# Kernel tuning notes

Hardware: AMD Instinct MI355X
Metric: run time of the kernel (lower is better)

## Reference

```python
import jax, jax.numpy as jnp
import numpy as np

N_NODES = 100000


def setup_inputs() -> dict:
    key = jax.random.key(0)
    k1, k2, k3, k4 = jax.random.split(key, 4)
    E = 1600000
    in_dim, out_dim = 256, 64
    h = jax.random.normal(k1, (N_NODES, in_dim), dtype=jnp.float32)
    src = jax.random.randint(k2, (E,), 0, N_NODES, dtype=jnp.int64)
    dst = jax.random.randint(k3, (E,), 0, N_NODES, dtype=jnp.int64)
    W = jax.random.normal(k4, (in_dim, out_dim), dtype=jnp.float32) * (1.0 / np.sqrt(in_dim))
    b = jnp.zeros((out_dim,), dtype=jnp.float32)
    return {"h": h, "src": src, "dst": dst, "W": W, "b": b}


def reference(h, src, dst, W, b):
    # dgl GraphConv, norm='both': out = D_in^{-1/2} A D_out^{-1/2} h W + b
    E = src.shape[0]
    ones = jnp.ones((E,), dtype=h.dtype)
    deg_out = jax.ops.segment_sum(ones, src, num_segments=N_NODES)  # out-degree of src nodes
    deg_in = jax.ops.segment_sum(ones, dst, num_segments=N_NODES)   # in-degree of dst nodes
    norm_src = jnp.clip(deg_out, 1.0, None) ** -0.5                  # [N]
    norm_dst = jnp.clip(deg_in, 1.0, None) ** -0.5                   # [N]
    # in_dim > out_dim: project first (as dgl does), then aggregate small features
    x = (h * norm_src[:, None]) @ W                                  # [N, out_dim]
    msgs = x[src]                                                    # [E, out_dim] gather
    agg = jax.ops.segment_sum(msgs, dst, num_segments=N_NODES)      # [N, out_dim] scatter-add
    out = agg * norm_dst[:, None] + b
    # ReLU; dropout is identity in eval mode
    return jax.nn.relu(out)
```

## Files before the change

kernel.cpp:

```cpp
#include <hip/hip_runtime.h>
#include <hip/hip_fp16.h>

#define N_NODES 100000
#define IN_DIM 256
#define OUT_DIM 64
#define NT 782
#define NB 256
#define SCHUNK 4096
#define SB ((NT * NB + SCHUNK - 1) / SCHUNK)
#define SCAN_M (NT * NB)

typedef _Float16 half8 __attribute__((ext_vector_type(8)));
typedef float f32x4 __attribute__((ext_vector_type(4)));

__global__ __launch_bounds__(256) void count_kernel(const int* __restrict__ src,
                                                    const int* __restrict__ dst,
                                                    int* __restrict__ CD, int* __restrict__ CS,
                                                    int E, int chunk) {
    __shared__ int hd[NT], hs[NT];
    const int t = threadIdx.x, blk = blockIdx.x;
    for (int i = t; i < NT; i += 256) { hd[i] = 0; hs[i] = 0; }
    __syncthreads();
    const int lo = blk * chunk;
    int hi = lo + chunk; if (hi > E) hi = E;
    for (int i = lo + t; i < hi; i += 256) {
        atomicAdd(&hd[dst[i] >> 7], 1);
        atomicAdd(&hs[src[i] >> 7], 1);
    }
    __syncthreads();
    for (int i = t; i < NT; i += 256) {
        CD[i * NB + blk] = hd[i];
        CS[i * NB + blk] = hs[i];
    }
}

__global__ __launch_bounds__(256) void scan_blocks_kernel(int* __restrict__ CD, int* __restrict__ CS,
                                                          int* __restrict__ BSD, int* __restrict__ BSS) {
    int cid = blockIdx.x;
    int* arr; int* bs;
    if (cid < SB) { arr = CD; bs = BSD; } else { arr = CS; bs = BSS; cid -= SB; }
    const int t = threadIdx.x;
    const int base = cid * SCHUNK + t * 16;
    int pre[16];
    int s = 0;
#pragma unroll
    for (int r = 0; r < 16; ++r) {
        int v = (base + r < SCAN_M) ? arr[base + r] : 0;
        pre[r] = s; s += v;
    }
    const int lane = t & 63;
    int incl = s;
#pragma unroll
    for (int off = 1; off < 64; off <<= 1) {
        int y = __shfl_up(incl, off);
        if (lane >= off) incl += y;
    }
    int wave_excl = incl - s;
    __shared__ int wtot[4];
    if (lane == 63) wtot[t >> 6] = incl;
    __syncthreads();
    int woff = 0;
    for (int w = 0; w < (t >> 6); ++w) woff += wtot[w];
    int bexcl = woff + wave_excl;
#pragma unroll
    for (int r = 0; r < 16; ++r)
        if (base + r < SCAN_M) arr[base + r] = bexcl + pre[r];
    if (t == 0) bs[cid] = wtot[0] + wtot[1] + wtot[2] + wtot[3];
}

__global__ void scan_sums_kernel(int* __restrict__ BSD, int* __restrict__ BSS) {
    const int t = threadIdx.x;
    const int lane = t & 63;
    int* bs = (t < 64) ? BSD : BSS;
    int v = (lane < SB) ? bs[lane] : 0;
    int incl = v;
#pragma unroll
    for (int off = 1; off < 64; off <<= 1) {
        int y = __shfl_up(incl, off);
        if (lane >= off) incl += y;
    }
    if (lane < SB) bs[lane] = incl - v;
}

__global__ __launch_bounds__(256) void scatter_kernel(const int* __restrict__ src,
                                                      const int* __restrict__ dst,
                                                      const int* __restrict__ CD, const int* __restrict__ CS,
                                                      const int* __restrict__ BSD, const int* __restrict__ BSS,
                                                      int* __restrict__ binnedD,
                                                      unsigned char* __restrict__ srcb,
                                                      int E, int chunk) {
    __shared__ int curD[NT], curS[NT];
    const int t = threadIdx.x, blk = blockIdx.x;
    for (int i = t; i < NT; i += 256) {
        int idx = i * NB + blk;
        curD[i] = CD[idx] + BSD[idx >> 12];
        curS[i] = CS[idx] + BSS[idx >> 12];
    }
    __syncthreads();
    const int lo = blk * chunk;
    int hi = lo + chunk; if (hi > E) hi = E;
    for (int i = lo + t; i < hi; i += 256) {
        int s = src[i], d = dst[i];
        int p = atomicAdd(&curD[d >> 7], 1);
        binnedD[p] = (s << 7) | (d & 127);
        int ps = atomicAdd(&curS[s >> 7], 1);
        srcb[ps] = (unsigned char)(s & 127);
    }
}

__global__ __launch_bounds__(256) void tile_kernel(const int* __restrict__ CD, const int* __restrict__ CS,
                                                   const int* __restrict__ BSD, const int* __restrict__ BSS,
                                                   const int* __restrict__ binnedD,
                                                   const unsigned char* __restrict__ srcb,
                                                   int* __restrict__ csr,
                                                   int* __restrict__ offs, int* __restrict__ cnt,
                                                   int* __restrict__ deg_out, int E) {
    __shared__ int h[128], cur[128];
    __shared__ int w0tot;
    const int bin = blockIdx.x, t = threadIdx.x, lane = t & 63;
    const int i0 = bin * NB;

    if (t < 128) h[t] = 0;
    __syncthreads();
    const int base = CD[i0] + BSD[i0 >> 12];
    const int next = (bin + 1 < NT) ? (CD[i0 + NB] + BSD[(i0 + NB) >> 12]) : E;
    const int m = next - base;
    for (int k = t; k < m; k += 256) atomicAdd(&h[binnedD[base + k] & 127], 1);
    __syncthreads();
    int v = (t < 128) ? h[t] : 0;
    int incl = v;
#pragma unroll
    for (int off = 1; off < 64; off <<= 1) {
        int y = __shfl_up(incl, off);
        if (lane >= off) incl += y;
    }
    if (t == 63) w0tot = incl;
    __syncthreads();
    int excl = incl - v + ((t >= 64 && t < 128) ? w0tot : 0);
    if (t < 128) {
        cur[t] = excl;
        int node = bin * 128 + t;
        if (node < N_NODES) { offs[node] = base + excl; cnt[node] = v; }
    }
    __syncthreads();
    for (int k = t; k < m; k += 256) {
        int rec = binnedD[base + k];
        int p = atomicAdd(&cur[rec & 127], 1);
        csr[base + p] = rec >> 7;
    }

    __syncthreads();
    if (t < 128) h[t] = 0;
    __syncthreads();
    const int sb = CS[i0] + BSS[i0 >> 12];
    const int sn = (bin + 1 < NT) ? (CS[i0 + NB] + BSS[(i0 + NB) >> 12]) : E;
    const int sm = sn - sb;
    for (int k = t; k < sm; k += 256) atomicAdd(&h[srcb[sb + k]], 1);
    __syncthreads();
    if (t < 128) {
        int node = bin * 128 + t;
        if (node < N_NODES) deg_out[node] = h[t];
    }
}

#define A_LD 136
__global__ __launch_bounds__(256) void gemm_kernel(const float* __restrict__ hmat,
                                                   const float* __restrict__ W,
                                                   const int* __restrict__ deg_out,
                                                   __half* __restrict__ xh) {
    __shared__ _Float16 sA[64 * A_LD];
    __shared__ _Float16 sB[64 * A_LD];
    const int t = threadIdx.x;
    const int lane = t & 63;
    const int w = t >> 6;
    const int row0 = blockIdx.x * 64;
    const int m0 = (w & 1) * 32;
    const int n0 = (w >> 1) * 32;

    f32x4 acc00 = {0.f, 0.f, 0.f, 0.f}, acc01 = {0.f, 0.f, 0.f, 0.f};
    f32x4 acc10 = {0.f, 0.f, 0.f, 0.f}, acc11 = {0.f, 0.f, 0.f, 0.f};

    for (int khalf = 0; khalf < 2; ++khalf) {
        const int k0 = khalf * 128;
        __syncthreads();
#pragma unroll
        for (int it = 0; it < 8; ++it) {
            int f = t + it * 256;
            int row = f >> 5;
            int c4 = f & 31;
            int grow = row0 + row; if (grow >= N_NODES) grow = N_NODES - 1;
            float4 v = *(const float4*)(hmat + (size_t)grow * IN_DIM + k0 + c4 * 4);
            _Float16 p[4];
            p[0] = (_Float16)v.x; p[1] = (_Float16)v.y;
            p[2] = (_Float16)v.z; p[3] = (_Float16)v.w;
            *(uint2*)&sA[row * A_LD + c4 * 4] = *(uint2*)p;
        }
        {
            int n = t & 63;
            int kk0 = (t >> 6) * 32;
#pragma unroll
            for (int kb = 0; kb < 8; ++kb) {
                _Float16 p[4];
#pragma unroll
                for (int u = 0; u < 4; ++u)
                    p[u] = (_Float16)W[(size_t)(k0 + kk0 + kb * 4 + u) * OUT_DIM + n];
                *(uint2*)&sB[n * A_LD + kk0 + kb * 4] = *(uint2*)p;
            }
        }
        __syncthreads();
#pragma unroll
        for (int kb = 0; kb < 4; ++kb) {
            int koff = kb * 32 + (lane >> 4) * 8;
            half8 a0 = *(const half8*)&sA[(m0 + (lane & 15)) * A_LD + koff];
            half8 a1 = *(const half8*)&sA[(m0 + 16 + (lane & 15)) * A_LD + koff];
            half8 b0 = *(const half8*)&sB[(n0 + (lane & 15)) * A_LD + koff];
            half8 b1 = *(const half8*)&sB[(n0 + 16 + (lane & 15)) * A_LD + koff];
            acc00 = __builtin_amdgcn_mfma_f32_16x16x32_f16(a0, b0, acc00, 0, 0, 0);
            acc01 = __builtin_amdgcn_mfma_f32_16x16x32_f16(a0, b1, acc01, 0, 0, 0);
            acc10 = __builtin_amdgcn_mfma_f32_16x16x32_f16(a1, b0, acc10, 0, 0, 0);
            acc11 = __builtin_amdgcn_mfma_f32_16x16x32_f16(a1, b1, acc11, 0, 0, 0);
        }
    }

    const int col16 = lane & 15;
    const int rq = (lane >> 4) * 4;
#pragma unroll
    for (int mi = 0; mi < 2; ++mi) {
        float nrm[4];
#pragma unroll
        for (int r = 0; r < 4; ++r) {
            int row = row0 + m0 + mi * 16 + rq + r;
            int d = (row < N_NODES) ? deg_out[row] : 1;
            nrm[r] = rsqrtf((float)(d < 1 ? 1 : d));
        }
#pragma unroll
        for (int ni = 0; ni < 2; ++ni) {
            const f32x4 a = (mi == 0) ? (ni == 0 ? acc00 : acc01)
                                      : (ni == 0 ? acc10 : acc11);
            int col = n0 + ni * 16 + col16;
#pragma unroll
            for (int r = 0; r < 4; ++r) {
                int row = row0 + m0 + mi * 16 + rq + r;
                if (row < N_NODES)
                    xh[(size_t)row * OUT_DIM + col] = __float2half(a[r] * nrm[r]);
            }
        }
    }
}

__global__ __launch_bounds__(256) void aggregate_kernel(const int* __restrict__ offs,
                                                        const int* __restrict__ cnt,
                                                        const int* __restrict__ csr,
                                                        const __half* __restrict__ xh,
                                                        const float* __restrict__ b,
                                                        float* __restrict__ out) {
    const int t = threadIdx.x;
    const int lane = t & 63;
    const int wid = t >> 6;
    const int node = blockIdx.x * 4 + wid;
    const int g = lane >> 3;
    const int c = lane & 7;

    const int start = offs[node];
    const int n = cnt[node];

    float acc[8] = {0.f, 0.f, 0.f, 0.f, 0.f, 0.f, 0.f, 0.f};
    for (int base = 0; base < n; base += 64) {
        int k = base + lane;
        int sidx = (k < n) ? csr[start + k] : 0;
        int m = n - base; if (m > 64) m = 64;
        for (int rb = 0; rb < m; rb += 32) {
            uint4 raw[4]; float wq[4];
#pragma unroll
            for (int q = 0; q < 4; ++q) {
                int e = rb + 8 * q + g;
                int s = __shfl(sidx, e);
                bool val = e < m;
                s = val ? s : 0;
                wq[q] = val ? 1.f : 0.f;
                raw[q] = *(const uint4*)(xh + (size_t)s * OUT_DIM + 8 * c);
            }
#pragma unroll
            for (int q = 0; q < 4; ++q) {
                const __half2* hp = (const __half2*)&raw[q];
#pragma unroll
                for (int p = 0; p < 4; ++p) {
                    float2 f = __half22float2(hp[p]);
                    acc[2 * p]     = fmaf(wq[q], f.x, acc[2 * p]);
                    acc[2 * p + 1] = fmaf(wq[q], f.y, acc[2 * p + 1]);
                }
            }
        }
    }

#pragma unroll
    for (int off = 8; off < 64; off <<= 1) {
#pragma unroll
        for (int p = 0; p < 8; ++p)
            acc[p] += __shfl_xor(acc[p], off);
    }

    if (g == 0) {
        float nrm = rsqrtf((float)(n < 1 ? 1 : n));
        float4 bv0 = *(const float4*)&b[c * 8];
        float4 bv1 = *(const float4*)&b[c * 8 + 4];
        float4 r0, r1;
        r0.x = fmaxf(fmaf(acc[0], nrm, bv0.x), 0.f);
        r0.y = fmaxf(fmaf(acc[1], nrm, bv0.y), 0.f);
        r0.z = fmaxf(fmaf(acc[2], nrm, bv0.z), 0.f);
        r0.w = fmaxf(fmaf(acc[3], nrm, bv0.w), 0.f);
        r1.x = fmaxf(fmaf(acc[4], nrm, bv1.x), 0.f);
        r1.y = fmaxf(fmaf(acc[5], nrm, bv1.y), 0.f);
        r1.z = fmaxf(fmaf(acc[6], nrm, bv1.z), 0.f);
        r1.w = fmaxf(fmaf(acc[7], nrm, bv1.w), 0.f);
        float4* orow = (float4*)(out + (size_t)node * OUT_DIM + c * 8);
        orow[0] = r0;
        orow[1] = r1;
    }
}

extern "C" void kernel_launch(void* const* d_in, const int* in_sizes, int n_in,
                              void* d_out, int out_size, void* d_ws, size_t ws_size,
                              hipStream_t stream) {
    const float* h   = (const float*)d_in[0];
    const int*   src = (const int*)d_in[1];
    const int*   dst = (const int*)d_in[2];
    const float* W   = (const float*)d_in[3];
    const float* b   = (const float*)d_in[4];
    float* out = (float*)d_out;
    const int E = in_sizes[1];
    const int chunk = (E + NB - 1) / NB;

    char* ws = (char*)d_ws;
    int*           CD      = (int*)(ws);
    int*           CS      = (int*)(ws + 800768);
    int*           BSD     = (int*)(ws + 1601536);
    int*           BSS     = (int*)(ws + 1601792);
    int*           binnedD = (int*)(ws + 1602048);
    unsigned char* srcb    = (unsigned char*)(ws + 8002048);
    int*           csr     = (int*)(ws + 9602048);
    int*           offs    = (int*)(ws + 16002048);
    int*           cntA    = (int*)(ws + 16402048);
    int*           deg_out = (int*)(ws + 16802048);
    __half*        xh      = (__half*)(ws + 17202048);

    count_kernel<<<NB, 256, 0, stream>>>(src, dst, CD, CS, E, chunk);
    scan_blocks_kernel<<<2 * SB, 256, 0, stream>>>(CD, CS, BSD, BSS);
    scan_sums_kernel<<<1, 128, 0, stream>>>(BSD, BSS);
    scatter_kernel<<<NB, 256, 0, stream>>>(src, dst, CD, CS, BSD, BSS, binnedD, srcb, E, chunk);
    tile_kernel<<<NT, 256, 0, stream>>>(CD, CS, BSD, BSS, binnedD, srcb, csr, offs, cntA, deg_out, E);
    gemm_kernel<<<(N_NODES + 63) / 64, 256, 0, stream>>>(h, W, deg_out, xh);
    aggregate_kernel<<<N_NODES / 4, 256, 0, stream>>>(offs, cntA, csr, xh, b, out);
}
```

Measured before the change: 294.8 us.

## Drop CSR build; aggregate per 128-node bin with LDS atomics

Removes the per-node CSR construction (tile_kernel), the source-side binning and the separate scan_sums kernel. Out-degree is now computed with global atomics in the scatter pass, and the block-sum scan is folded into its consumers. Aggregation runs one block per 128-destination bin, reading binned records directly and accumulating fp32 rows in shared memory with LDS atomics. This cuts launches and global memory passes, at the cost of heavy shared-memory atomic traffic and a large LDS footprint per block, which may limit occupancy.

```diff
diff --git a/kernel.cpp b/kernel.cpp
--- a/kernel.cpp
+++ b/kernel.cpp
@@ -13,39 +13,33 @@
 typedef _Float16 half8 __attribute__((ext_vector_type(8)));
 typedef float f32x4 __attribute__((ext_vector_type(4)));
 
-__global__ __launch_bounds__(256) void count_kernel(const int* __restrict__ src,
-                                                    const int* __restrict__ dst,
-                                                    int* __restrict__ CD, int* __restrict__ CS,
+__global__ __launch_bounds__(256) void count_kernel(const int* __restrict__ dst,
+                                                    int* __restrict__ CD,
+                                                    int* __restrict__ deg_out,
                                                     int E, int chunk) {
-    __shared__ int hd[NT], hs[NT];
+    __shared__ int hd[NT];
     const int t = threadIdx.x, blk = blockIdx.x;
-    for (int i = t; i < NT; i += 256) { hd[i] = 0; hs[i] = 0; }
+    for (int i = t; i < NT; i += 256) hd[i] = 0;
+    for (int i = blk * 256 + t; i < N_NODES; i += NB * 256) deg_out[i] = 0;
     __syncthreads();
     const int lo = blk * chunk;
     int hi = lo + chunk; if (hi > E) hi = E;
-    for (int i = lo + t; i < hi; i += 256) {
+    for (int i = lo + t; i < hi; i += 256)
         atomicAdd(&hd[dst[i] >> 7], 1);
-        atomicAdd(&hs[src[i] >> 7], 1);
-    }
-    __syncthreads();
-    for (int i = t; i < NT; i += 256) {
+    __syncthreads();
+    for (int i = t; i < NT; i += 256)
         CD[i * NB + blk] = hd[i];
-        CS[i * NB + blk] = hs[i];
-    }
-}
-
-__global__ __launch_bounds__(256) void scan_blocks_kernel(int* __restrict__ CD, int* __restrict__ CS,
-                                                          int* __restrict__ BSD, int* __restrict__ BSS) {
-    int cid = blockIdx.x;
-    int* arr; int* bs;
-    if (cid < SB) { arr = CD; bs = BSD; } else { arr = CS; bs = BSS; cid -= SB; }
+}
+
+__global__ __launch_bounds__(256) void scan_blocks_kernel(int* __restrict__ CD, int* __restrict__ BS) {
+    const int cid = blockIdx.x;
     const int t = threadIdx.x;
     const int base = cid * SCHUNK + t * 16;
     int pre[16];
     int s = 0;
 #pragma unroll
     for (int r = 0; r < 16; ++r) {
-        int v = (base + r < SCAN_M) ? arr[base + r] : 0;
+        int v = (base + r < SCAN_M) ? CD[base + r] : 0;
         pre[r] = s; s += v;
     }
     const int lane = t & 63;
@@ -64,102 +58,43 @@
     int bexcl = woff + wave_excl;
 #pragma unroll
     for (int r = 0; r < 16; ++r)
-        if (base + r < SCAN_M) arr[base + r] = bexcl + pre[r];
-    if (t == 0) bs[cid] = wtot[0] + wtot[1] + wtot[2] + wtot[3];
-}
-
-__global__ void scan_sums_kernel(int* __restrict__ BSD, int* __restrict__ BSS) {
-    const int t = threadIdx.x;
-    const int lane = t & 63;
-    int* bs = (t < 64) ? BSD : BSS;
-    int v = (lane < SB) ? bs[lane] : 0;
-    int incl = v;
-#pragma unroll
-    for (int off = 1; off < 64; off <<= 1) {
-        int y = __shfl_up(incl, off);
-        if (lane >= off) incl += y;
-    }
-    if (lane < SB) bs[lane] = incl - v;
+        if (base + r < SCAN_M) CD[base + r] = bexcl + pre[r];
+    if (t == 0) BS[cid] = wtot[0] + wtot[1] + wtot[2] + wtot[3];
 }
 
 __global__ __launch_bounds__(256) void scatter_kernel(const int* __restrict__ src,
                                                       const int* __restrict__ dst,
-                                                      const int* __restrict__ CD, const int* __restrict__ CS,
-                                                      const int* __restrict__ BSD, const int* __restrict__ BSS,
+                                                      const int* __restrict__ CD,
+                                                      const int* __restrict__ BS,
                                                       int* __restrict__ binnedD,
-                                                      unsigned char* __restrict__ srcb,
+                                                      int* __restrict__ deg_out,
                                                       int E, int chunk) {
-    __shared__ int curD[NT], curS[NT];
+    __shared__ int curD[NT];
+    __shared__ int sBS[64];
     const int t = threadIdx.x, blk = blockIdx.x;
+    if (t < 64) {
+        int v = (t < SB) ? BS[t] : 0;
+        int incl = v;
+#pragma unroll
+        for (int off = 1; off < 64; off <<= 1) {
+            int y = __shfl_up(incl, off);
+            if (t >= off) incl += y;
+        }
+        sBS[t] = incl - v;
+    }
+    __syncthreads();
     for (int i = t; i < NT; i += 256) {
         int idx = i * NB + blk;
-        curD[i] = CD[idx] + BSD[idx >> 12];
-        curS[i] = CS[idx] + BSS[idx >> 12];
+        curD[i] = CD[idx] + sBS[idx >> 12];
     }
     __syncthreads();
     const int lo = blk * chunk;
     int hi = lo + chunk; if (hi > E) hi = E;
     for (int i = lo + t; i < hi; i += 256) {
         int s = src[i], d = dst[i];
+        atomicAdd(&deg_out[s], 1);
         int p = atomicAdd(&curD[d >> 7], 1);
         binnedD[p] = (s << 7) | (d & 127);
-        int ps = atomicAdd(&curS[s >> 7], 1);
-        srcb[ps] = (unsigned char)(s & 127);
-    }
-}
-
-__global__ __launch_bounds__(256) void tile_kernel(const int* __restrict__ CD, const int* __restrict__ CS,
-                                                   const int* __restrict__ BSD, const int* __restrict__ BSS,
-                                                   const int* __restrict__ binnedD,
-                                                   const unsigned char* __restrict__ srcb,
-                                                   int* __restrict__ csr,
-                                                   int* __restrict__ offs, int* __restrict__ cnt,
-                                                   int* __restrict__ deg_out, int E) {
-    __shared__ int h[128], cur[128];
-    __shared__ int w0tot;
-    const int bin = blockIdx.x, t = threadIdx.x, lane = t & 63;
-    const int i0 = bin * NB;
-
-    if (t < 128) h[t] = 0;
-    __syncthreads();
-    const int base = CD[i0] + BSD[i0 >> 12];
-    const int next = (bin + 1 < NT) ? (CD[i0 + NB] + BSD[(i0 + NB) >> 12]) : E;
-    const int m = next - base;
-    for (int k = t; k < m; k += 256) atomicAdd(&h[binnedD[base + k] & 127], 1);
-    __syncthreads();
-    int v = (t < 128) ? h[t] : 0;
-    int incl = v;
-#pragma unroll
-    for (int off = 1; off < 64; off <<= 1) {
-        int y = __shfl_up(incl, off);
-        if (lane >= off) incl += y;
-    }
-    if (t == 63) w0tot = incl;
-    __syncthreads();
-    int excl = incl - v + ((t >= 64 && t < 128) ? w0tot : 0);
-    if (t < 128) {
-        cur[t] = excl;
-        int node = bin * 128 + t;
-        if (node < N_NODES) { offs[node] = base + excl; cnt[node] = v; }
-    }
-    __syncthreads();
-    for (int k = t; k < m; k += 256) {
-        int rec = binnedD[base + k];
-        int p = atomicAdd(&cur[rec & 127], 1);
-        csr[base + p] = rec >> 7;
-    }
-
-    __syncthreads();
-    if (t < 128) h[t] = 0;
-    __syncthreads();
-    const int sb = CS[i0] + BSS[i0 >> 12];
-    const int sn = (bin + 1 < NT) ? (CS[i0 + NB] + BSS[(i0 + NB) >> 12]) : E;
-    const int sm = sn - sb;
-    for (int k = t; k < sm; k += 256) atomicAdd(&h[srcb[sb + k]], 1);
-    __syncthreads();
-    if (t < 128) {
-        int node = bin * 128 + t;
-        if (node < N_NODES) deg_out[node] = h[t];
     }
 }
 
@@ -248,74 +183,84 @@
     }
 }
 
-__global__ __launch_bounds__(256) void aggregate_kernel(const int* __restrict__ offs,
-                                                        const int* __restrict__ cnt,
-                                                        const int* __restrict__ csr,
+#define AGG_LD 65
+__global__ __launch_bounds__(256) void aggregate_kernel(const int* __restrict__ CD,
+                                                        const int* __restrict__ BS,
+                                                        const int* __restrict__ binnedD,
                                                         const __half* __restrict__ xh,
                                                         const float* __restrict__ b,
-                                                        float* __restrict__ out) {
-    const int t = threadIdx.x;
-    const int lane = t & 63;
-    const int wid = t >> 6;
-    const int node = blockIdx.x * 4 + wid;
-    const int g = lane >> 3;
-    const int c = lane & 7;
-
-    const int start = offs[node];
-    const int n = cnt[node];
-
-    float acc[8] = {0.f, 0.f, 0.f, 0.f, 0.f, 0.f, 0.f, 0.f};
-    for (int base = 0; base < n; base += 64) {
-        int k = base + lane;
-        int sidx = (k < n) ? csr[start + k] : 0;
-        int m = n - base; if (m > 64) m = 64;
-        for (int rb = 0; rb < m; rb += 32) {
-            uint4 raw[4]; float wq[4];
-#pragma unroll
-            for (int q = 0; q < 4; ++q) {
-                int e = rb + 8 * q + g;
-                int s = __shfl(sidx, e);
-                bool val = e < m;
-                s = val ? s : 0;
-                wq[q] = val ? 1.f : 0.f;
-                raw[q] = *(const uint4*)(xh + (size_t)s * OUT_DIM + 8 * c);
-            }
-#pragma unroll
-            for (int q = 0; q < 4; ++q) {
-                const __half2* hp = (const __half2*)&raw[q];
+                                                        float* __restrict__ out, int E) {
+    __shared__ float acc[128 * AGG_LD];
+    __shared__ int cnt[128];
+    __shared__ int sBS[64];
+    const int t = threadIdx.x, bin = blockIdx.x;
+    if (t < 64) {
+        int v = (t < SB) ? BS[t] : 0;
+        int incl = v;
+#pragma unroll
+        for (int off = 1; off < 64; off <<= 1) {
+            int y = __shfl_up(incl, off);
+            if (t >= off) incl += y;
+        }
+        sBS[t] = incl - v;
+    }
+    for (int i = t; i < 128 * AGG_LD; i += 256) acc[i] = 0.f;
+    if (t < 128) cnt[t] = 0;
+    __syncthreads();
+
+    const int i0 = bin * NB;
+    const int base = CD[i0] + sBS[i0 >> 12];
+    const int next = (bin + 1 < NT) ? (CD[i0 + NB] + sBS[(i0 + NB) >> 12]) : E;
+
+    const int c = t & 7;
+    const int eo = t >> 3;
+    for (int k0 = base; k0 < next; k0 += 32 * 4) {
+        int recs[4]; uint4 v[4];
+#pragma unroll
+        for (int u = 0; u < 4; ++u) {
+            int k = k0 + u * 32 + eo;
+            recs[u] = (k < next) ? binnedD[k] : -1;
+        }
+#pragma unroll
+        for (int u = 0; u < 4; ++u) {
+            int s = (recs[u] >= 0) ? (recs[u] >> 7) : 0;
+            v[u] = *(const uint4*)(xh + (size_t)s * OUT_DIM + c * 8);
+        }
+#pragma unroll
+        for (int u = 0; u < 4; ++u) {
+            if (recs[u] >= 0) {
+                int d = recs[u] & 127;
+                float* row = &acc[d * AGG_LD + c * 8];
+                const __half2* hp = (const __half2*)&v[u];
 #pragma unroll
                 for (int p = 0; p < 4; ++p) {
                     float2 f = __half22float2(hp[p]);
-                    acc[2 * p]     = fmaf(wq[q], f.x, acc[2 * p]);
-                    acc[2 * p + 1] = fmaf(wq[q], f.y, acc[2 * p + 1]);
+                    atomicAdd(row + 2 * p,     f.x);
+                    atomicAdd(row + 2 * p + 1, f.y);
                 }
+                if (c == 0) atomicAdd(&cnt[d], 1);
             }
         }
     }
-
-#pragma unroll
-    for (int off = 8; off < 64; off <<= 1) {
-#pragma unroll
-        for (int p = 0; p < 8; ++p)
-            acc[p] += __shfl_xor(acc[p], off);
-    }
-
-    if (g == 0) {
-        float nrm = rsqrtf((float)(n < 1 ? 1 : n));
-        float4 bv0 = *(const float4*)&b[c * 8];
-        float4 bv1 = *(const float4*)&b[c * 8 + 4];
-        float4 r0, r1;
-        r0.x = fmaxf(fmaf(acc[0], nrm, bv0.x), 0.f);
-        r0.y = fmaxf(fmaf(acc[1], nrm, bv0.y), 0.f);
-        r0.z = fmaxf(fmaf(acc[2], nrm, bv0.z), 0.f);
-        r0.w = fmaxf(fmaf(acc[3], nrm, bv0.w), 0.f);
-        r1.x = fmaxf(fmaf(acc[4], nrm, bv1.x), 0.f);
-        r1.y = fmaxf(fmaf(acc[5], nrm, bv1.y), 0.f);
-        r1.z = fmaxf(fmaf(acc[6], nrm, bv1.z), 0.f);
-        r1.w = fmaxf(fmaf(acc[7], nrm, bv1.w), 0.f);
-        float4* orow = (float4*)(out + (size_t)node * OUT_DIM + c * 8);
-        orow[0] = r0;
-        orow[1] = r1;
+    __syncthreads();
+
+    const int node0 = bin * 128;
+#pragma unroll
+    for (int i = t; i < 128 * 16; i += 256) {
+        int r = i >> 4, q = i & 15;
+        int node = node0 + r;
+        if (node < N_NODES) {
+            int n = cnt[r];
+            float nrm = rsqrtf((float)(n < 1 ? 1 : n));
+            const float* a = &acc[r * AGG_LD + q * 4];
+            float4 bv = *(const float4*)(b + q * 4);
+            float4 o;
+            o.x = fmaxf(fmaf(a[0], nrm, bv.x), 0.f);
+            o.y = fmaxf(fmaf(a[1], nrm, bv.y), 0.f);
+            o.z = fmaxf(fmaf(a[2], nrm, bv.z), 0.f);
+            o.w = fmaxf(fmaf(a[3], nrm, bv.w), 0.f);
+            *(float4*)(out + (size_t)node * OUT_DIM + q * 4) = o;
+        }
     }
 }
 
@@ -332,23 +277,15 @@
     const int chunk = (E + NB - 1) / NB;
 
     char* ws = (char*)d_ws;
-    int*           CD      = (int*)(ws);
-    int*           CS      = (int*)(ws + 800768);
-    int*           BSD     = (int*)(ws + 1601536);
-    int*           BSS     = (int*)(ws + 1601792);
-    int*           binnedD = (int*)(ws + 1602048);
-    unsigned char* srcb    = (unsigned char*)(ws + 8002048);
-    int*           csr     = (int*)(ws + 9602048);
-    int*           offs    = (int*)(ws + 16002048);
-    int*           cntA    = (int*)(ws + 16402048);
-    int*           deg_out = (int*)(ws + 16802048);
-    __half*        xh      = (__half*)(ws + 17202048);
-
-    count_kernel<<<NB, 256, 0, stream>>>(src, dst, CD, CS, E, chunk);
-    scan_blocks_kernel<<<2 * SB, 256, 0, stream>>>(CD, CS, BSD, BSS);
-    scan_sums_kernel<<<1, 128, 0, stream>>>(BSD, BSS);
-    scatter_kernel<<<NB, 256, 0, stream>>>(src, dst, CD, CS, BSD, BSS, binnedD, srcb, E, chunk);
-    tile_kernel<<<NT, 256, 0, stream>>>(CD, CS, BSD, BSS, binnedD, srcb, csr, offs, cntA, deg_out, E);
+    int*    CD      = (int*)(ws);
+    int*    BS      = (int*)(ws + 800768);
+    int*    binnedD = (int*)(ws + 801024);
+    int*    deg_out = (int*)(ws + 7201024);
+    __half* xh      = (__half*)(ws + 7601024);
+
+    count_kernel<<<NB, 256, 0, stream>>>(dst, CD, deg_out, E, chunk);
+    scan_blocks_kernel<<<SB, 256, 0, stream>>>(CD, BS);
+    scatter_kernel<<<NB, 256, 0, stream>>>(src, dst, CD, BS, binnedD, deg_out, E, chunk);
     gemm_kernel<<<(N_NODES + 63) / 64, 256, 0, stream>>>(h, W, deg_out, xh);
-    aggregate_kernel<<<N_NODES / 4, 256, 0, stream>>>(offs, cntA, csr, xh, b, out);
-}
+    aggregate_kernel<<<NT, 256, 0, stream>>>(CD, BS, binnedD, xh, b, out, E);
+}
```

After: 944.6 us. 3.2x slower.
